# Performance work log

Measured on AMD Instinct MI355X. Metric: run time of the kernel, lower is better.

## Reference

```python
import jax, jax.numpy as jnp
import numpy as np

B, N, D, H, CD = 1, 512, 256, 8, 3
HD = D // H
HID = int(D * 4.0 * (2.0 / 3.0))  # 682, SwiGLU hidden


def _ln(x, w, b, eps=1e-5):
    mu = jnp.mean(x, axis=-1, keepdims=True)
    var = jnp.var(x, axis=-1, keepdims=True)
    return (x - mu) / jnp.sqrt(var + eps) * w + b


def setup_inputs() -> dict:
    key = jax.random.key(0)
    ks = jax.random.split(key, 24)
    g = lambda i, shape, fan: jax.random.normal(ks[i], shape, jnp.float32) * (1.0 / np.sqrt(fan))
    return {
        "x": jax.random.normal(ks[0], (B, N, D), jnp.float32),
        "coords": jax.random.normal(ks[1], (B, N, CD), jnp.float32),
        "ln1_w": jnp.ones((D,), jnp.float32), "ln1_b": jnp.zeros((D,), jnp.float32),
        "ln2_w": jnp.ones((D,), jnp.float32), "ln2_b": jnp.zeros((D,), jnp.float32),
        "qkv_w": g(2, (3 * D, D), D), "qkv_b": jnp.zeros((3 * D,), jnp.float32),
        "rb1_w": g(3, (D, CD), CD), "rb1_b": jnp.zeros((D,), jnp.float32),
        "rb2_w": g(4, (H, D), D), "rb2_b": jnp.zeros((H,), jnp.float32),
        "rv1_w": g(5, (D, CD), CD), "rv1_b": jnp.zeros((D,), jnp.float32),
        "rv2_w": g(6, (D, D), D), "rv2_b": jnp.zeros((D,), jnp.float32),
        "ffn_w1": g(7, (HID, D), D), "ffn_b1": jnp.zeros((HID,), jnp.float32),
        "ffn_w2": g(8, (HID, D), D), "ffn_b2": jnp.zeros((HID,), jnp.float32),
        "ffn_w3": g(9, (D, HID), HID), "ffn_b3": jnp.zeros((D,), jnp.float32),
    }


def _forward(x, coords, ln1_w, ln1_b, ln2_w, ln2_b, qkv_w, qkv_b,
             rb1_w, rb1_b, rb2_w, rb2_b, rv1_w, rv1_b, rv2_w, rv2_b,
             ffn_w1, ffn_b1, ffn_w2, ffn_b2, ffn_w3, ffn_b3):
    silu = jax.nn.silu
    xn = _ln(x, ln1_w, ln1_b)
    qkv = xn @ qkv_w.T + qkv_b                       # [B,N,3D]
    q, k, v = jnp.split(qkv, 3, axis=-1)
    tohead = lambda t: t.reshape(B, N, H, HD).transpose(0, 2, 1, 3)  # [B,H,N,hd]
    qh, kh, vh = tohead(q), tohead(k), tohead(v)

    rel = coords[:, :, None, :] - coords[:, None, :, :]              # [B,N,N,3]
    rel_bias = silu(rel @ rb1_w.T + rb1_b) @ rb2_w.T + rb2_b         # [B,N,N,H]
    rel_bias = rel_bias.transpose(0, 3, 1, 2)                        # [B,H,N,N]
    rel_value = silu(rel @ rv1_w.T + rv1_b) @ rv2_w.T + rv2_b        # [B,N,N,D]
    rel_value = rel_value.reshape(B, N, N, H, HD).transpose(0, 3, 1, 2, 4)  # [B,H,N,N,hd]

    scores = jnp.einsum('bhid,bhjd->bhij', qh, kh) / np.sqrt(float(HD))
    weights = jax.nn.softmax(scores + rel_bias, axis=-1)             # [B,H,N,N]
    context = jnp.einsum('bhij,bhjd->bhid', weights, vh) \
            + jnp.einsum('bhij,bhijd->bhid', weights, rel_value)
    attn_out = context.transpose(0, 2, 1, 3).reshape(B, N, D)

    x = x + attn_out
    xn2 = _ln(x, ln2_w, ln2_b)
    ffn = (silu(xn2 @ ffn_w1.T + ffn_b1) * (xn2 @ ffn_w2.T + ffn_b2)) @ ffn_w3.T + ffn_b3
    return x + ffn


def reference(x, coords, ln1_w, ln1_b, ln2_w, ln2_b, qkv_w, qkv_b,
              rb1_w, rb1_b, rb2_w, rb2_b, rv1_w, rv1_b, rv2_w, rv2_b,
              ffn_w1, ffn_b1, ffn_w2, ffn_b2, ffn_w3, ffn_b3):
    return _forward(x, coords, ln1_w, ln1_b, ln2_w, ln2_b, qkv_w, qkv_b,
                    rb1_w, rb1_b, rb2_w, rb2_b, rv1_w, rv1_b, rv2_w, rv2_b,
                    ffn_w1, ffn_b1, ffn_w2, ffn_b2, ffn_w3, ffn_b3)
```

## Files before the change

kernel.cpp:

```cpp
#include <hip/hip_runtime.h>


#define NN 512
#define DD 256
#define HH 8
#define HIDN 682
#define QKSCALE 0.17677669529663687f

#define OFF_XN     0
#define OFF_X2     0
#define OFF_Q      131072
#define OFF_W3P    131072
#define OFF_VPF    262144
#define OFF_RV2T   393216
#define OFF_RB2F   458752
#define OFF_KF     460800
#define OFF_PBF    526336
#define OFF_H1     526336
#define OFF_PVF    788480
#define OFF_QKVP   1050624
#define OFF_XN2    1050624
#define OFF_W12P   1247232

typedef float  f32x4  __attribute__((ext_vector_type(4)));
typedef short  bf16x8 __attribute__((ext_vector_type(8)));
typedef unsigned int u32;
typedef unsigned short ushortt;

static __device__ __forceinline__ float wredSum(float v){
#pragma unroll
  for (int o = 1; o < 64; o <<= 1) v += __shfl_xor(v, o, 64);
  return v;
}
static __device__ __forceinline__ float wredMax(float v){
#pragma unroll
  for (int o = 1; o < 64; o <<= 1) v = fmaxf(v, __shfl_xor(v, o, 64));
  return v;
}
static __device__ __forceinline__ float fsilu(float x){
  return x * __builtin_amdgcn_rcpf(1.0f + __expf(-x));
}
static __device__ __forceinline__ u32 cvtpk(float lo, float hi){
  u32 d; asm("v_cvt_pk_bf16_f32 %0, %1, %2" : "=v"(d) : "v"(lo), "v"(hi));
  return d;
}
static __device__ __forceinline__ float us2f(ushortt u){
  union{u32 u; float f;} c; c.u = ((u32)u) << 16; return c.f;
}
static __device__ __forceinline__ bf16x8 mkfrag(u32 a, u32 b, u32 c, u32 d){
  union{u32 u[4]; bf16x8 s;} f; f.u[0]=a; f.u[1]=b; f.u[2]=c; f.u[3]=d; return f.s;
}
static __device__ __forceinline__ float dot4(float4 a, float4 b){
  return a.x*b.x + a.y*b.y + a.z*b.z + a.w*b.w;
}

__global__ __launch_bounds__(256) void k1_prep(
    const float* __restrict__ x, const float* __restrict__ coords,
    const float* __restrict__ ln1_w, const float* __restrict__ ln1_b,
    const float* __restrict__ rb1_w, const float* __restrict__ rv1_w,
    const float* __restrict__ rv2_w, const float* __restrict__ rb2_w,
    const float* __restrict__ qkv_w, const float* __restrict__ w1,
    const float* __restrict__ w2, float* __restrict__ ws)
{
  __shared__ float r4[4];
  const int b = blockIdx.x, t = threadIdx.x;
  if (b < 512) {
    const int lane = t & 63, wid = t >> 6;
    const float v = x[b*DD + t];
    float s = wredSum(v);
    if (lane == 0) r4[wid] = s;
    __syncthreads();
    const float mu = (r4[0]+r4[1]+r4[2]+r4[3]) * (1.0f/DD);
    const float d = v - mu;
    float s2 = wredSum(d*d);
    __syncthreads();
    if (lane == 0) r4[wid] = s2;
    __syncthreads();
    const float var = (r4[0]+r4[1]+r4[2]+r4[3]) * (1.0f/DD);
    ws[OFF_XN + b*DD + t] = d*rsqrtf(var + 1e-5f)*ln1_w[t] + ln1_b[t];
  } else if (b < 768) {
    const int e = b - 512;
    ws[OFF_RV2T + e*DD + t] = rv2_w[t*DD + e];
  } else if (b == 768) {
    u32* RBF = (u32*)(ws + OFF_RB2F);
    const int l = t & 63, lm = l & 15, lg = (l >> 4) & 3, kq = t >> 6;
#pragma unroll
    for (int g = 0; g < 2; ++g) {
      const int ks = g*4 + kq;
      u32 dw[4];
#pragma unroll
      for (int dd = 0; dd < 4; ++dd) {
        const int e0 = ks*32 + lg*8 + 2*dd;
        const float f0 = (lm < HH) ? rb2_w[lm*DD + e0]     : 0.f;
        const float f1 = (lm < HH) ? rb2_w[lm*DD + e0 + 1] : 0.f;
        dw[dd] = cvtpk(f0, f1);
      }
      uint4 q4; q4.x = dw[0]; q4.y = dw[1]; q4.z = dw[2]; q4.w = dw[3];
      *(uint4*)(RBF + (ks*64 + l)*4) = q4;
    }
  } else if (b < 833) {
    float4* dst = (float4*)(ws + OFF_PBF);
#pragma unroll
    for (int k = 0; k < 4; ++k) {
      const int L4 = (b - 769)*1024 + k*256 + t;
      const int lm = L4 & 15, q = (L4>>4)&3, lg = (L4>>6)&3, ks = (L4>>8)&7, jt = L4>>11;
      const int j = jt*16 + lm, e0 = ks*32 + lg*8 + q*2;
      const float c0 = coords[j*3], c1 = coords[j*3+1], c2 = coords[j*3+2];
      const float p0 = c0*rb1_w[e0*3]   + c1*rb1_w[e0*3+1] + c2*rb1_w[e0*3+2];
      const float p1 = c0*rb1_w[e0*3+3] + c1*rb1_w[e0*3+4] + c2*rb1_w[e0*3+5];
      dst[L4] = make_float4(p0, __expf(p0), p1, __expf(p1));
    }
  } else if (b < 897) {
    float4* dst = (float4*)(ws + OFF_PVF);
#pragma unroll
    for (int k = 0; k < 4; ++k) {
      const int L4 = (b - 833)*1024 + k*256 + t;
      const int lm = L4 & 15, q = (L4>>4)&3, lg = (L4>>6)&3, ks = (L4>>8)&15, et = L4>>12;
      const int e = et*16 + lm, j0 = ks*32 + lg*8 + q*2;
      const float w0 = rv1_w[e*3], w1_ = rv1_w[e*3+1], w2_ = rv1_w[e*3+2];
      const float p0 = coords[j0*3]*w0 + coords[j0*3+1]*w1_ + coords[j0*3+2]*w2_;
      const float p1 = coords[j0*3+3]*w0 + coords[j0*3+4]*w1_ + coords[j0*3+5]*w2_;
      dst[L4] = make_float4(p0, __expf(p0), p1, __expf(p1));
    }
  } else if (b < 945) {
    float4* dst = (float4*)(ws + OFF_QKVP);
#pragma unroll
    for (int k = 0; k < 4; ++k) {
      const int L4 = (b - 897)*1024 + k*256 + t;
      const int O = L4 % 768, k4 = L4 / 768;
      dst[L4] = *(const float4*)(qkv_w + O*DD + k4*4);
    }
  } else {
    float4* dst = (float4*)(ws + OFF_W12P);
    for (int L4 = (b - 945)*256 + t; L4 < 87296; L4 += 88*256) {
      const int pr = L4 & 1, rest = L4 >> 1;
      const int O = rest % 682, k4 = rest / 682;
      dst[L4] = *(const float4*)((pr ? w2 : w1) + O*DD + k4*4);
    }
  }
}

__global__ __launch_bounds__(256) void k2_qkv(
    float* __restrict__ ws, const float* __restrict__ qkv_b)
{
  const int i0 = blockIdx.x*2, rep = blockIdx.y, t = threadIdx.x;
  const int O = rep*DD + t;
  const float4* xn4 = (const float4*)(ws + OFF_XN);
  const float4* wp4 = (const float4*)(ws + OFF_QKVP);
  float a0 = qkv_b[O], a1 = a0;
  for (int k4 = 0; k4 < 64; ++k4) {
    const float4 w = wp4[k4*768 + O];
    const float4 x0 = xn4[i0*64 + k4];
    const float4 x1 = xn4[i0*64 + 64 + k4];
    a0 += dot4(x0, w);
    a1 += dot4(x1, w);
  }
  if (rep == 0) {
    ws[OFF_Q + i0*DD + t] = a0;
    ws[OFF_Q + (i0+1)*DD + t] = a1;
  } else if (rep == 1) {
    u32* KF = (u32*)(ws + OFF_KF);
    const int c = t;
    const float p0 = __shfl_xor(a0, 1);
    const float p1 = __shfl_xor(a1, 1);
    if ((c & 1) == 0) {
      const int hq = c >> 5, lgk = (c >> 3) & 3, dw = (c & 7) >> 1;
      const int jt0_ = i0 >> 4, lm0 = i0 & 15;
      KF[(((jt0_*8 + hq)*4 + lgk)*16 + lm0)*4 + dw] = cvtpk(a0, p0);
      const int j1 = i0 + 1, jt1_ = j1 >> 4, lm1 = j1 & 15;
      KF[(((jt1_*8 + hq)*4 + lgk)*16 + lm1)*4 + dw] = cvtpk(a1, p1);
    }
  } else {
    ws[OFF_VPF + i0*DD + t] = a0;
    ws[OFF_VPF + (i0+1)*DD + t] = a1;
  }
}

__global__ __launch_bounds__(512, 4) void k3_attn(
    const float* __restrict__ x, const float* __restrict__ coords,
    const float* __restrict__ rb1_w, const float* __restrict__ rb1_b,
    const float* __restrict__ rv1_w, const float* __restrict__ rv1_b,
    const float* __restrict__ rv2_b, const float* __restrict__ ln2_w,
    const float* __restrict__ ln2_b, float* __restrict__ ws)
{
  __shared__ __align__(16) float aI[DD], eIl[DD], pvIl[DD], evIl[DD], qI[DD];
  __shared__ __align__(16) float uni[4352];
  __shared__ __align__(16) float GhL[HH*258];
  __shared__ __align__(16) float c1h[2*DD];
  __shared__ float red[8];
  float* swl = uni;
  ushortt* wtl = (ushortt*)uni;

  const int i = blockIdx.x, t = threadIdx.x;
  const int lane = t & 63, wid = t >> 6, lm = lane & 15, lg = lane >> 4;
  const float* qbuf = ws + OFF_Q;
  const float4* PBF4 = (const float4*)(ws + OFF_PBF);
  const float4* PVF4 = (const float4*)(ws + OFF_PVF);
  const uint4*  KF4  = (const uint4*)(ws + OFF_KF);
  const u32*    RBF  = (const u32*)(ws + OFF_RB2F);
  const float*  rv2t = ws + OFF_RV2T;
  const float*  vpf  = ws + OFF_VPF;

  if (t < DD) {
    const float c0 = coords[i*3], c1 = coords[i*3+1], c2 = coords[i*3+2];
    const float a  = c0*rb1_w[t*3] + c1*rb1_w[t*3+1] + c2*rb1_w[t*3+2] + rb1_b[t];
    aI[t] = a;  eIl[t] = __expf(-a);
    const float pv = c0*rv1_w[t*3] + c1*rv1_w[t*3+1] + c2*rv1_w[t*3+2] + rv1_b[t];
    pvIl[t] = pv; evIl[t] = __expf(-pv);
    qI[t] = qbuf[i*DD + t];
  }
  __syncthreads();

  {
    f32x4 z4 = {0.f,0.f,0.f,0.f};
    f32x4 acc[4] = {z4,z4,z4,z4};
    const int jt0 = wid*4;
    for (int ks = 0; ks < 8; ++ks) {
      const uint4 bd = *(const uint4*)(RBF + (ks*64 + lane)*4);
      const bf16x8 bfr = mkfrag(bd.x, bd.y, bd.z, bd.w);
      const float4 aA0 = *(const float4*)&aI[ks*32 + lg*8];
      const float4 aA1 = *(const float4*)&aI[ks*32 + lg*8 + 4];
      const float4 eA0 = *(const float4*)&eIl[ks*32 + lg*8];
      const float4 eA1 = *(const float4*)&eIl[ks*32 + lg*8 + 4];
#pragma unroll
      for (int jt = 0; jt < 4; ++jt) {
        const float4* src = PBF4 + ((jt0+jt)*32 + ks*4 + lg)*64 + lm;
        const float4 g0 = src[0], g1 = src[16], g2 = src[32], g3 = src[48];
        const float s0 = (aA0.x-g0.x)*__builtin_amdgcn_rcpf(fmaf(eA0.x,g0.y,1.f));
        const float s1 = (aA0.y-g0.z)*__builtin_amdgcn_rcpf(fmaf(eA0.y,g0.w,1.f));
        const float s2 = (aA0.z-g1.x)*__builtin_amdgcn_rcpf(fmaf(eA0.z,g1.y,1.f));
        const float s3 = (aA0.w-g1.z)*__builtin_amdgcn_rcpf(fmaf(eA0.w,g1.w,1.f));
        const float s4 = (aA1.x-g2.x)*__builtin_amdgcn_rcpf(fmaf(eA1.x,g2.y,1.f));
        const float s5 = (aA1.y-g2.z)*__builtin_amdgcn_rcpf(fmaf(eA1.y,g2.w,1.f));
        const float s6 = (aA1.z-g3.x)*__builtin_amdgcn_rcpf(fmaf(eA1.z,g3.y,1.f));
        const float s7 = (aA1.w-g3.z)*__builtin_amdgcn_rcpf(fmaf(eA1.w,g3.w,1.f));
        const bf16x8 afr = mkfrag(cvtpk(s0,s1), cvtpk(s2,s3), cvtpk(s4,s5), cvtpk(s6,s7));
        acc[jt] = __builtin_amdgcn_mfma_f32_16x16x32_bf16(afr, bfr, acc[jt], 0, 0, 0);
      }
    }
#pragma unroll
    for (int hq = 0; hq < 8; ++hq) {
      const float4 q0 = *(const float4*)&qI[hq*32 + lg*8];
      const float4 q1 = *(const float4*)&qI[hq*32 + lg*8 + 4];
      const float m = (lm == hq) ? QKSCALE : 0.f;
      const bf16x8 bfr = mkfrag(cvtpk(q0.x*m, q0.y*m), cvtpk(q0.z*m, q0.w*m),
                                cvtpk(q1.x*m, q1.y*m), cvtpk(q1.z*m, q1.w*m));
#pragma unroll
      for (int jt = 0; jt < 4; ++jt) {
        const uint4 ad = KF4[(((jt0+jt)*8 + hq)*4 + lg)*16 + lm];
        const bf16x8 afr = mkfrag(ad.x, ad.y, ad.z, ad.w);
        acc[jt] = __builtin_amdgcn_mfma_f32_16x16x32_bf16(afr, bfr, acc[jt], 0, 0, 0);
      }
    }
    if (lm < HH) {
#pragma unroll
      for (int jt = 0; jt < 4; ++jt)
#pragma unroll
        for (int g = 0; g < 4; ++g)
          swl[lm*513 + wid*64 + jt*16 + lg*4 + g] = acc[jt][g];
    }
  }
  __syncthreads();

  float sv[8];
  {
    float mm = -3.4e38f;
#pragma unroll
    for (int r = 0; r < 8; ++r) { sv[r] = swl[wid*513 + lane + r*64]; mm = fmaxf(mm, sv[r]); }
    mm = wredMax(mm);
    float sum = 0.f;
#pragma unroll
    for (int r = 0; r < 8; ++r) { sv[r] = __expf(sv[r] - mm); sum += sv[r]; }
    sum = wredSum(sum);
    const float rz = __builtin_amdgcn_rcpf(sum);
#pragma unroll
    for (int r = 0; r < 8; ++r) sv[r] *= rz;
  }
  __syncthreads();
#pragma unroll
  for (int r = 0; r < 8; ++r)
    wtl[(lane + r*64)*17 + wid] = (ushortt)(cvtpk(sv[r], 0.f) & 0xFFFFu);
  __syncthreads();

  {
    f32x4 z4 = {0.f,0.f,0.f,0.f};
    f32x4 accB0 = z4, accB1 = z4;
    const int et0 = wid*2;
    const int eR0 = et0*16 + lm, eR1 = eR0 + 16;
    const float aV0 = pvIl[eR0], eV0 = evIl[eR0];
    const float aV1 = pvIl[eR1], eV1 = evIl[eR1];
    for (int ks = 0; ks < 16; ++ks) {
      ushortt wv[8];
#pragma unroll
      for (int r = 0; r < 8; ++r) wv[r] = wtl[(ks*32 + lg*8 + r)*17 + lm];
      const bf16x8 wfr = mkfrag((u32)wv[0] | ((u32)wv[1] << 16),
                                (u32)wv[2] | ((u32)wv[3] << 16),
                                (u32)wv[4] | ((u32)wv[5] << 16),
                                (u32)wv[6] | ((u32)wv[7] << 16));
      {
        const float4* src = PVF4 + ((et0*16 + ks)*4 + lg)*64 + lm;
        const float4 g0 = src[0], g1 = src[16], g2 = src[32], g3 = src[48];
        const float s0 = (aV0-g0.x)*__builtin_amdgcn_rcpf(fmaf(eV0,g0.y,1.f));
        const float s1 = (aV0-g0.z)*__builtin_amdgcn_rcpf(fmaf(eV0,g0.w,1.f));
        const float s2 = (aV0-g1.x)*__builtin_amdgcn_rcpf(fmaf(eV0,g1.y,1.f));
        const float s3 = (aV0-g1.z)*__builtin_amdgcn_rcpf(fmaf(eV0,g1.w,1.f));
        const float s4 = (aV0-g2.x)*__builtin_amdgcn_rcpf(fmaf(eV0,g2.y,1.f));
        const float s5 = (aV0-g2.z)*__builtin_amdgcn_rcpf(fmaf(eV0,g2.w,1.f));
        const float s6 = (aV0-g3.x)*__builtin_amdgcn_rcpf(fmaf(eV0,g3.y,1.f));
        const float s7 = (aV0-g3.z)*__builtin_amdgcn_rcpf(fmaf(eV0,g3.w,1.f));
        const bf16x8 afr = mkfrag(cvtpk(s0,s1), cvtpk(s2,s3), cvtpk(s4,s5), cvtpk(s6,s7));
        accB0 = __builtin_amdgcn_mfma_f32_16x16x32_bf16(afr, wfr, accB0, 0, 0, 0);
      }
      {
        const float4* src = PVF4 + (((et0+1)*16 + ks)*4 + lg)*64 + lm;
        const float4 g0 = src[0], g1 = src[16], g2 = src[32], g3 = src[48];
        const float s0 = (aV1-g0.x)*__builtin_amdgcn_rcpf(fmaf(eV1,g0.y,1.f));
        const float s1 = (aV1-g0.z)*__builtin_amdgcn_rcpf(fmaf(eV1,g0.w,1.f));
        const float s2 = (aV1-g1.x)*__builtin_amdgcn_rcpf(fmaf(eV1,g1.y,1.f));
        const float s3 = (aV1-g1.z)*__builtin_amdgcn_rcpf(fmaf(eV1,g1.w,1.f));
        const float s4 = (aV1-g2.x)*__builtin_amdgcn_rcpf(fmaf(eV1,g2.y,1.f));
        const float s5 = (aV1-g2.z)*__builtin_amdgcn_rcpf(fmaf(eV1,g2.w,1.f));
        const float s6 = (aV1-g3.x)*__builtin_amdgcn_rcpf(fmaf(eV1,g3.y,1.f));
        const float s7 = (aV1-g3.z)*__builtin_amdgcn_rcpf(fmaf(eV1,g3.w,1.f));
        const bf16x8 afr = mkfrag(cvtpk(s0,s1), cvtpk(s2,s3), cvtpk(s4,s5), cvtpk(s6,s7));
        accB1 = __builtin_amdgcn_mfma_f32_16x16x32_bf16(afr, wfr, accB1, 0, 0, 0);
      }
    }
    if (lm < HH) {
#pragma unroll
      for (int g = 0; g < 4; ++g) {
        GhL[lm*258 + et0*16 + lg*4 + g]     = accB0[g];
        GhL[lm*258 + (et0+1)*16 + lg*4 + g] = accB1[g];
      }
    }
  }

  {
    const int c = t & 255, half = t >> 8, h = c >> 5;
    float a0 = 0.f;
    for (int j = half*256; j < half*256 + 256; ++j)
      a0 += us2f(wtl[j*17 + h]) * vpf[j*DD + c];
    c1h[half*DD + c] = a0;
  }
  __syncthreads();

  float x2v = 0.f;
  if (t < DD) {
    const int c = t, h = c >> 5;
    float a0 = 0.f;
    for (int e = 0; e < DD; ++e) a0 += GhL[h*258 + e] * rv2t[e*DD + c];
    x2v = x[i*DD + c] + c1h[c] + c1h[DD + c] + a0 + rv2_b[c];
  }
  float s = wredSum(x2v);
  if (lane == 0) red[wid] = s;
  __syncthreads();
  const float mu = (red[0]+red[1]+red[2]+red[3]) * (1.0f/DD);
  const float dv = (t < DD) ? (x2v - mu) : 0.f;
  float s2 = wredSum(dv*dv);
  __syncthreads();
  if (lane == 0) red[wid] = s2;
  __syncthreads();
  const float var = (red[0]+red[1]+red[2]+red[3]) * (1.0f/DD);
  const float rstd = rsqrtf(var + 1e-5f);
  if (t < DD) {
    ws[OFF_X2  + i*DD + t] = x2v;
    ws[OFF_XN2 + i*DD + t] = (x2v - mu)*rstd*ln2_w[t] + ln2_b[t];
  }
}

__global__ __launch_bounds__(256) void k4_ffn1(
    float* __restrict__ ws, const float* __restrict__ b1,
    const float* __restrict__ b2, const float* __restrict__ w3)
{
  const int rep = blockIdx.y, t = threadIdx.x;
  if (rep == 3) {
    float2* dst = (float2*)(ws + OFF_W3P);
    for (int L2 = blockIdx.x*256 + t; L2 < 87296; L2 += 256*256) {
      const int c = L2 & 255, k2i = L2 >> 8;
      dst[L2] = *(const float2*)(w3 + c*HIDN + 2*k2i);
    }
    return;
  }
  const int i0 = blockIdx.x*2;
  const int O = rep*DD + t;
  if (O >= HIDN) return;
  const float4* xn4 = (const float4*)(ws + OFF_XN2);
  const float4* wp4 = (const float4*)(ws + OFF_W12P);
  float a10 = b1[O], a11 = a10;
  float a20 = b2[O], a21 = a20;
  for (int k4 = 0; k4 < 64; ++k4) {
    const float4 u = wp4[(k4*HIDN + O)*2];
    const float4 v = wp4[(k4*HIDN + O)*2 + 1];
    const float4 x0 = xn4[i0*64 + k4];
    const float4 x1 = xn4[i0*64 + 64 + k4];
    a10 += dot4(x0, u); a20 += dot4(x0, v);
    a11 += dot4(x1, u); a21 += dot4(x1, v);
  }
  ws[OFF_H1 + i0*HIDN + O]     = fsilu(a10)*a20;
  ws[OFF_H1 + (i0+1)*HIDN + O] = fsilu(a11)*a21;
}

__global__ __launch_bounds__(256) void k5_ffn2(
    const float* __restrict__ ws, const float* __restrict__ b3, float* __restrict__ out)
{
  const int i = blockIdx.x, c = threadIdx.x;
  const float2* wp2 = (const float2*)(ws + OFF_W3P);
  const float2* h2  = (const float2*)(ws + OFF_H1 + i*HIDN);
  float acc = b3[c] + ws[OFF_X2 + i*DD + c];
  for (int k = 0; k < 341; ++k) {
    const float2 w = wp2[k*DD + c];
    const float2 h = h2[k];
    acc += h.x*w.x + h.y*w.y;
  }
  out[i*DD + c] = acc;
}

extern "C" void kernel_launch(void* const* d_in, const int* in_sizes, int n_in,
                              void* d_out, int out_size, void* d_ws, size_t ws_size,
                              hipStream_t stream) {
  (void)in_sizes; (void)n_in; (void)out_size; (void)ws_size;
  const float* x      = (const float*)d_in[0];
  const float* coords = (const float*)d_in[1];
  const float* ln1_w  = (const float*)d_in[2];
  const float* ln1_b  = (const float*)d_in[3];
  const float* ln2_w  = (const float*)d_in[4];
  const float* ln2_b  = (const float*)d_in[5];
  const float* qkv_w  = (const float*)d_in[6];
  const float* qkv_b  = (const float*)d_in[7];
  const float* rb1_w  = (const float*)d_in[8];
  const float* rb1_b  = (const float*)d_in[9];
  const float* rb2_w  = (const float*)d_in[10];
  const float* rv1_w  = (const float*)d_in[12];
  const float* rv1_b  = (const float*)d_in[13];
  const float* rv2_w  = (const float*)d_in[14];
  const float* rv2_b  = (const float*)d_in[15];
  const float* ffn_w1 = (const float*)d_in[16];
  const float* ffn_b1 = (const float*)d_in[17];
  const float* ffn_w2 = (const float*)d_in[18];
  const float* ffn_b2 = (const float*)d_in[19];
  const float* ffn_w3 = (const float*)d_in[20];
  const float* ffn_b3 = (const float*)d_in[21];
  float* ws  = (float*)d_ws;
  float* out = (float*)d_out;

  k1_prep<<<1033, 256, 0, stream>>>(x, coords, ln1_w, ln1_b, rb1_w, rv1_w,
                                    rv2_w, rb2_w, qkv_w, ffn_w1, ffn_w2, ws);
  k2_qkv<<<dim3(256, 3), 256, 0, stream>>>(ws, qkv_b);
  k3_attn<<<NN, 512, 0, stream>>>(x, coords, rb1_w, rb1_b, rv1_w, rv1_b, rv2_b,
                                  ln2_w, ln2_b, ws);
  k4_ffn1<<<dim3(256, 4), 256, 0, stream>>>(ws, ffn_b1, ffn_b2, ffn_w3);
  k5_ffn2<<<NN, 256, 0, stream>>>(ws, ffn_b3, out);
}
```

Before: 259.6 us.

## Split attention into scores, softmax, context kernels with fp16 packing and row blocking

The monolithic per-row attention kernel becomes three kernels. The first computes bias and QK scores for four query rows per block, sharing fragment loads across rows. The second applies softmax over packed fp16 weights, and the third computes the value and rel-value context for two rows per block, doing the rv2 projection with MFMA instead of a scalar loop. Precomputed coordinate projections are stored as fp16 without the exp half, Q is pre-scaled into bf16, V is stored transposed in bf16, and the FFN weight packing moves to its own kernel. The FFN kernels now process 16 rows per block so each weight load is reused across rows. This adds launches and lowers intermediate precision, which risks larger numerical error.

After: 336.8 us. 1.3x slower.

```diff
diff --git a/kernel.cpp b/kernel.cpp
--- a/kernel.cpp
+++ b/kernel.cpp
@@ -7,25 +7,26 @@
 #define HIDN 682
 #define QKSCALE 0.17677669529663687f
 
-#define OFF_XN     0
-#define OFF_X2     0
-#define OFF_Q      131072
-#define OFF_W3P    131072
-#define OFF_VPF    262144
-#define OFF_RV2T   393216
-#define OFF_RB2F   458752
-#define OFF_KF     460800
-#define OFF_PBF    526336
-#define OFF_H1     526336
-#define OFF_PVF    788480
-#define OFF_QKVP   1050624
-#define OFF_XN2    1050624
-#define OFF_W12P   1247232
+#define OFF_QB    0
+#define OFF_PB    65536
+#define OFF_X2    0
+#define OFF_KF    131072
+#define OFF_RB2F  196608
+#define OFF_XN2   131072
+#define OFF_RV2F  262144
+#define OFF_VT    294912
+#define OFF_PV    360448
+#define OFF_WB    425984
+#define OFF_XN    425984
+#define OFF_QKVP  557056
+#define OFF_W12P  425984
+#define OFF_W3P   775168
+#define OFF_H1    949760
 
 typedef float  f32x4  __attribute__((ext_vector_type(4)));
 typedef short  bf16x8 __attribute__((ext_vector_type(8)));
+typedef __fp16 fp16x2 __attribute__((ext_vector_type(2)));
 typedef unsigned int u32;
-typedef unsigned short ushortt;
 
 static __device__ __forceinline__ float wredSum(float v){
 #pragma unroll
@@ -44,8 +45,15 @@
   u32 d; asm("v_cvt_pk_bf16_f32 %0, %1, %2" : "=v"(d) : "v"(lo), "v"(hi));
   return d;
 }
-static __device__ __forceinline__ float us2f(ushortt u){
-  union{u32 u; float f;} c; c.u = ((u32)u) << 16; return c.f;
+static __device__ __forceinline__ u32 pkf16(float lo, float hi){
+  fp16x2 r = __builtin_amdgcn_cvt_pkrtz(lo, hi);
+  union{fp16x2 h; u32 u;} c; c.h = r; return c.u;
+}
+static __device__ __forceinline__ float f16lo(u32 d){
+  union{unsigned short s; __fp16 h;} c; c.s = (unsigned short)(d & 0xffffu); return (float)c.h;
+}
+static __device__ __forceinline__ float f16hi(u32 d){
+  union{unsigned short s; __fp16 h;} c; c.s = (unsigned short)(d >> 16); return (float)c.h;
 }
 static __device__ __forceinline__ bf16x8 mkfrag(u32 a, u32 b, u32 c, u32 d){
   union{u32 u[4]; bf16x8 s;} f; f.u[0]=a; f.u[1]=b; f.u[2]=c; f.u[3]=d; return f.s;
@@ -59,8 +67,7 @@
     const float* __restrict__ ln1_w, const float* __restrict__ ln1_b,
     const float* __restrict__ rb1_w, const float* __restrict__ rv1_w,
     const float* __restrict__ rv2_w, const float* __restrict__ rb2_w,
-    const float* __restrict__ qkv_w, const float* __restrict__ w1,
-    const float* __restrict__ w2, float* __restrict__ ws)
+    const float* __restrict__ qkv_w, float* __restrict__ ws)
 {
   __shared__ float r4[4];
   const int b = blockIdx.x, t = threadIdx.x;
@@ -78,64 +85,78 @@
     __syncthreads();
     const float var = (r4[0]+r4[1]+r4[2]+r4[3]) * (1.0f/DD);
     ws[OFF_XN + b*DD + t] = d*rsqrtf(var + 1e-5f)*ln1_w[t] + ln1_b[t];
-  } else if (b < 768) {
-    const int e = b - 512;
-    ws[OFF_RV2T + e*DD + t] = rv2_w[t*DD + e];
-  } else if (b == 768) {
+  } else if (b < 528) {
+    u32* PB32 = (u32*)(ws + OFF_PB);
+#pragma unroll
+    for (int k = 0; k < 4; ++k) {
+      const int L = (b-512)*1024 + k*256 + t;
+      const int jt = L >> 9, ks = (L >> 6) & 7, ln = L & 63;
+      const int lmm = ln & 15, lgg = ln >> 4;
+      const int j = jt*16 + lmm, e0 = ks*32 + lgg*8;
+      const float c0 = coords[j*3], c1 = coords[j*3+1], c2 = coords[j*3+2];
+      float p[8];
+#pragma unroll
+      for (int r = 0; r < 8; ++r)
+        p[r] = c0*rb1_w[(e0+r)*3] + c1*rb1_w[(e0+r)*3+1] + c2*rb1_w[(e0+r)*3+2];
+      uint4 q; q.x = pkf16(p[0],p[1]); q.y = pkf16(p[2],p[3]);
+      q.z = pkf16(p[4],p[5]); q.w = pkf16(p[6],p[7]);
+      *(uint4*)(PB32 + (size_t)L*4) = q;
+    }
+  } else if (b < 544) {
+    u32* PV32 = (u32*)(ws + OFF_PV);
+#pragma unroll
+    for (int k = 0; k < 4; ++k) {
+      const int L = (b-528)*1024 + k*256 + t;
+      const int et = L >> 10, ks = (L >> 6) & 15, ln = L & 63;
+      const int lmm = ln & 15, lgg = ln >> 4;
+      const int e = et*16 + lmm, j0 = ks*32 + lgg*8;
+      const float w0 = rv1_w[e*3], w1 = rv1_w[e*3+1], w2 = rv1_w[e*3+2];
+      float p[8];
+#pragma unroll
+      for (int r = 0; r < 8; ++r)
+        p[r] = coords[(j0+r)*3]*w0 + coords[(j0+r)*3+1]*w1 + coords[(j0+r)*3+2]*w2;
+      uint4 q; q.x = pkf16(p[0],p[1]); q.y = pkf16(p[2],p[3]);
+      q.z = pkf16(p[4],p[5]); q.w = pkf16(p[6],p[7]);
+      *(uint4*)(PV32 + (size_t)L*4) = q;
+    }
+  } else if (b < 552) {
+    u32* RV32 = (u32*)(ws + OFF_RV2F);
+#pragma unroll
+    for (int k = 0; k < 4; ++k) {
+      const int L = (b-544)*1024 + k*256 + t;
+      const int mt = L >> 9, ks2 = (L >> 6) & 7, ln = L & 63;
+      const int lmm = ln & 15, lgg = ln >> 4;
+      const int c = mt*16 + lmm, e0 = ks2*32 + lgg*8;
+      const float4 f0 = *(const float4*)(rv2_w + c*DD + e0);
+      const float4 f1 = *(const float4*)(rv2_w + c*DD + e0 + 4);
+      uint4 q; q.x = cvtpk(f0.x,f0.y); q.y = cvtpk(f0.z,f0.w);
+      q.z = cvtpk(f1.x,f1.y); q.w = cvtpk(f1.z,f1.w);
+      *(uint4*)(RV32 + (size_t)L*4) = q;
+    }
+  } else if (b == 552) {
     u32* RBF = (u32*)(ws + OFF_RB2F);
-    const int l = t & 63, lm = l & 15, lg = (l >> 4) & 3, kq = t >> 6;
+    const int l = t & 63, lmm = l & 15, lgg = (l >> 4) & 3, kq = t >> 6;
 #pragma unroll
     for (int g = 0; g < 2; ++g) {
       const int ks = g*4 + kq;
       u32 dw[4];
 #pragma unroll
       for (int dd = 0; dd < 4; ++dd) {
-        const int e0 = ks*32 + lg*8 + 2*dd;
-        const float f0 = (lm < HH) ? rb2_w[lm*DD + e0]     : 0.f;
-        const float f1 = (lm < HH) ? rb2_w[lm*DD + e0 + 1] : 0.f;
+        const int e0 = ks*32 + lgg*8 + 2*dd;
+        const float f0 = (lmm < HH) ? rb2_w[lmm*DD + e0]     : 0.f;
+        const float f1 = (lmm < HH) ? rb2_w[lmm*DD + e0 + 1] : 0.f;
         dw[dd] = cvtpk(f0, f1);
       }
       uint4 q4; q4.x = dw[0]; q4.y = dw[1]; q4.z = dw[2]; q4.w = dw[3];
       *(uint4*)(RBF + (ks*64 + l)*4) = q4;
     }
-  } else if (b < 833) {
-    float4* dst = (float4*)(ws + OFF_PBF);
+  } else {
+    float4* dst = (float4*)(ws + OFF_QKVP);
 #pragma unroll
     for (int k = 0; k < 4; ++k) {
-      const int L4 = (b - 769)*1024 + k*256 + t;
-      const int lm = L4 & 15, q = (L4>>4)&3, lg = (L4>>6)&3, ks = (L4>>8)&7, jt = L4>>11;
-      const int j = jt*16 + lm, e0 = ks*32 + lg*8 + q*2;
-      const float c0 = coords[j*3], c1 = coords[j*3+1], c2 = coords[j*3+2];
-      const float p0 = c0*rb1_w[e0*3]   + c1*rb1_w[e0*3+1] + c2*rb1_w[e0*3+2];
-      const float p1 = c0*rb1_w[e0*3+3] + c1*rb1_w[e0*3+4] + c2*rb1_w[e0*3+5];
-      dst[L4] = make_float4(p0, __expf(p0), p1, __expf(p1));
-    }
-  } else if (b < 897) {
-    float4* dst = (float4*)(ws + OFF_PVF);
-#pragma unroll
-    for (int k = 0; k < 4; ++k) {
-      const int L4 = (b - 833)*1024 + k*256 + t;
-      const int lm = L4 & 15, q = (L4>>4)&3, lg = (L4>>6)&3, ks = (L4>>8)&15, et = L4>>12;
-      const int e = et*16 + lm, j0 = ks*32 + lg*8 + q*2;
-      const float w0 = rv1_w[e*3], w1_ = rv1_w[e*3+1], w2_ = rv1_w[e*3+2];
-      const float p0 = coords[j0*3]*w0 + coords[j0*3+1]*w1_ + coords[j0*3+2]*w2_;
-      const float p1 = coords[j0*3+3]*w0 + coords[j0*3+4]*w1_ + coords[j0*3+5]*w2_;
-      dst[L4] = make_float4(p0, __expf(p0), p1, __expf(p1));
-    }
-  } else if (b < 945) {
-    float4* dst = (float4*)(ws + OFF_QKVP);
-#pragma unroll
-    for (int k = 0; k < 4; ++k) {
-      const int L4 = (b - 897)*1024 + k*256 + t;
+      const int L4 = (b - 553)*1024 + k*256 + t;
       const int O = L4 % 768, k4 = L4 / 768;
       dst[L4] = *(const float4*)(qkv_w + O*DD + k4*4);
-    }
-  } else {
-    float4* dst = (float4*)(ws + OFF_W12P);
-    for (int L4 = (b - 945)*256 + t; L4 < 87296; L4 += 88*256) {
-      const int pr = L4 & 1, rest = L4 >> 1;
-      const int O = rest % 682, k4 = rest / 682;
-      dst[L4] = *(const float4*)((pr ? w2 : w1) + O*DD + k4*4);
     }
   }
 }
@@ -156,263 +177,349 @@
     a1 += dot4(x1, w);
   }
   if (rep == 0) {
-    ws[OFF_Q + i0*DD + t] = a0;
-    ws[OFF_Q + (i0+1)*DD + t] = a1;
+    u32* QB = (u32*)(ws + OFF_QB);
+    const float s0 = a0*QKSCALE, s1 = a1*QKSCALE;
+    const float p0 = __shfl_xor(s0, 1);
+    const float p1 = __shfl_xor(s1, 1);
+    if ((t & 1) == 0) {
+      QB[i0*128 + (t >> 1)]     = cvtpk(s0, p0);
+      QB[(i0+1)*128 + (t >> 1)] = cvtpk(s1, p1);
+    }
   } else if (rep == 1) {
     u32* KF = (u32*)(ws + OFF_KF);
-    const int c = t;
     const float p0 = __shfl_xor(a0, 1);
     const float p1 = __shfl_xor(a1, 1);
-    if ((c & 1) == 0) {
-      const int hq = c >> 5, lgk = (c >> 3) & 3, dw = (c & 7) >> 1;
+    if ((t & 1) == 0) {
+      const int hq = t >> 5, lgk = (t >> 3) & 3, dw = (t & 7) >> 1;
       const int jt0_ = i0 >> 4, lm0 = i0 & 15;
       KF[(((jt0_*8 + hq)*4 + lgk)*16 + lm0)*4 + dw] = cvtpk(a0, p0);
       const int j1 = i0 + 1, jt1_ = j1 >> 4, lm1 = j1 & 15;
       KF[(((jt1_*8 + hq)*4 + lgk)*16 + lm1)*4 + dw] = cvtpk(a1, p1);
     }
   } else {
-    ws[OFF_VPF + i0*DD + t] = a0;
-    ws[OFF_VPF + (i0+1)*DD + t] = a1;
-  }
-}
-
-__global__ __launch_bounds__(512, 4) void k3_attn(
+    u32* VT = (u32*)(ws + OFF_VT);
+    VT[t*256 + (i0 >> 1)] = cvtpk(a0, a1);
+  }
+}
+
+__global__ __launch_bounds__(256, 2) void k3a_scores(
+    const float* __restrict__ coords, const float* __restrict__ rb1_w,
+    const float* __restrict__ rb1_b, float* __restrict__ ws)
+{
+  __shared__ __align__(16) float aI4[4][DD];
+  __shared__ __align__(16) float eI4[4][DD];
+  const int bx = blockIdx.x, t = threadIdx.x;
+  const int it = bx >> 2, jq = bx & 3, i0 = it*4;
+  const int lane = t & 63, w = t >> 6, lm = lane & 15, lg = lane >> 4;
+  {
+    const float w0 = rb1_w[t*3], w1 = rb1_w[t*3+1], w2 = rb1_w[t*3+2], bb = rb1_b[t];
+#pragma unroll
+    for (int i = 0; i < 4; ++i) {
+      const float a = coords[(i0+i)*3]*w0 + coords[(i0+i)*3+1]*w1
+                    + coords[(i0+i)*3+2]*w2 + bb;
+      aI4[i][t] = a; eI4[i][t] = __expf(-a);
+    }
+  }
+  __syncthreads();
+  const uint4* PBu = (const uint4*)(ws + OFF_PB);
+  const uint4* KFu = (const uint4*)(ws + OFF_KF);
+  const uint4* QBu = (const uint4*)(ws + OFF_QB);
+  const u32*   RBF = (const u32*)(ws + OFF_RB2F);
+  const int jtA = jq*8 + w*2;
+  f32x4 z = {0,0,0,0};
+  f32x4 acc[2][4] = {{z,z,z,z},{z,z,z,z}};
+  for (int ks = 0; ks < 8; ++ks) {
+    const uint4 bd = *(const uint4*)(RBF + (ks*64 + lane)*4);
+    const bf16x8 bfr = mkfrag(bd.x,bd.y,bd.z,bd.w);
+    float4 aA[4][2], eA[4][2];
+#pragma unroll
+    for (int i = 0; i < 4; ++i) {
+      aA[i][0] = *(const float4*)&aI4[i][ks*32 + lg*8];
+      aA[i][1] = *(const float4*)&aI4[i][ks*32 + lg*8 + 4];
+      eA[i][0] = *(const float4*)&eI4[i][ks*32 + lg*8];
+      eA[i][1] = *(const float4*)&eI4[i][ks*32 + lg*8 + 4];
+    }
+#pragma unroll
+    for (int j2 = 0; j2 < 2; ++j2) {
+      const uint4 pd = PBu[((jtA+j2)*8 + ks)*64 + lane];
+      float p[8], ep[8];
+      p[0]=f16lo(pd.x); p[1]=f16hi(pd.x); p[2]=f16lo(pd.y); p[3]=f16hi(pd.y);
+      p[4]=f16lo(pd.z); p[5]=f16hi(pd.z); p[6]=f16lo(pd.w); p[7]=f16hi(pd.w);
+#pragma unroll
+      for (int r = 0; r < 8; ++r) ep[r] = __expf(p[r]);
+#pragma unroll
+      for (int i = 0; i < 4; ++i) {
+        const float* aa = (const float*)&aA[i][0];
+        const float* ee = (const float*)&eA[i][0];
+        float s[8];
+#pragma unroll
+        for (int r = 0; r < 8; ++r)
+          s[r] = (aa[r] - p[r]) * __builtin_amdgcn_rcpf(fmaf(ee[r], ep[r], 1.f));
+        const bf16x8 afr = mkfrag(cvtpk(s[0],s[1]), cvtpk(s[2],s[3]),
+                                  cvtpk(s[4],s[5]), cvtpk(s[6],s[7]));
+        acc[j2][i] = __builtin_amdgcn_mfma_f32_16x16x32_bf16(afr, bfr, acc[j2][i], 0,0,0);
+      }
+    }
+  }
+#pragma unroll
+  for (int hq = 0; hq < 8; ++hq) {
+    uint4 qd[4];
+#pragma unroll
+    for (int i = 0; i < 4; ++i) qd[i] = QBu[(i0+i)*32 + hq*4 + lg];
+    const bool sel = (lm == hq);
+#pragma unroll
+    for (int j2 = 0; j2 < 2; ++j2) {
+      const uint4 kd = KFu[((jtA+j2)*8 + hq)*64 + lane];
+      const bf16x8 kfr = mkfrag(kd.x,kd.y,kd.z,kd.w);
+#pragma unroll
+      for (int i = 0; i < 4; ++i) {
+        const bf16x8 qfr = mkfrag(sel?qd[i].x:0u, sel?qd[i].y:0u,
+                                  sel?qd[i].z:0u, sel?qd[i].w:0u);
+        acc[j2][i] = __builtin_amdgcn_mfma_f32_16x16x32_bf16(kfr, qfr, acc[j2][i], 0,0,0);
+      }
+    }
+  }
+  u32* WB = (u32*)(ws + OFF_WB);
+  if (lm < HH) {
+#pragma unroll
+    for (int j2 = 0; j2 < 2; ++j2) {
+      const int jt = jtA + j2, j0 = jt*16 + lg*4;
+      const int ksw = j0 >> 5, rr = j0 & 31, lgw = rr >> 3, d0 = (rr & 7) >> 1;
+#pragma unroll
+      for (int i = 0; i < 4; ++i) {
+        const int idx = (((i0+i)*16 + ksw)*32 + lgw*8 + lm)*4 + d0;
+        uint2 st; st.x = pkf16(acc[j2][i][0], acc[j2][i][1]);
+        st.y = pkf16(acc[j2][i][2], acc[j2][i][3]);
+        *(uint2*)(WB + idx) = st;
+      }
+    }
+  }
+}
+
+__global__ __launch_bounds__(256) void k3b_softmax(float* __restrict__ ws)
+{
+  const int i = blockIdx.x, t = threadIdx.x;
+  const int lane = t & 63, w4 = t >> 6;
+  u32* WB = (u32*)(ws + OFF_WB);
+  const int ks = lane >> 2, d = lane & 3;
+#pragma unroll
+  for (int hh = 0; hh < 2; ++hh) {
+    const int h = w4 + hh*4;
+    u32 dv[4]; float v[8];
+#pragma unroll
+    for (int lg = 0; lg < 4; ++lg) {
+      dv[lg] = WB[(i*16 + ks)*128 + (lg*8 + h)*4 + d];
+      v[lg*2]   = f16lo(dv[lg]);
+      v[lg*2+1] = f16hi(dv[lg]);
+    }
+    float m = v[0];
+#pragma unroll
+    for (int r = 1; r < 8; ++r) m = fmaxf(m, v[r]);
+    m = wredMax(m);
+    float s = 0.f;
+#pragma unroll
+    for (int r = 0; r < 8; ++r) { v[r] = __expf(v[r] - m); s += v[r]; }
+    s = wredSum(s);
+    const float rz = __builtin_amdgcn_rcpf(s);
+#pragma unroll
+    for (int lg = 0; lg < 4; ++lg)
+      WB[(i*16 + ks)*128 + (lg*8 + h)*4 + d] = cvtpk(v[lg*2]*rz, v[lg*2+1]*rz);
+  }
+}
+
+__global__ __launch_bounds__(512, 2) void k3c_ctx(
     const float* __restrict__ x, const float* __restrict__ coords,
-    const float* __restrict__ rb1_w, const float* __restrict__ rb1_b,
     const float* __restrict__ rv1_w, const float* __restrict__ rv1_b,
     const float* __restrict__ rv2_b, const float* __restrict__ ln2_w,
     const float* __restrict__ ln2_b, float* __restrict__ ws)
 {
-  __shared__ __align__(16) float aI[DD], eIl[DD], pvIl[DD], evIl[DD], qI[DD];
-  __shared__ __align__(16) float uni[4352];
-  __shared__ __align__(16) float GhL[HH*258];
-  __shared__ __align__(16) float c1h[2*DD];
-  __shared__ float red[8];
-  float* swl = uni;
-  ushortt* wtl = (ushortt*)uni;
-
-  const int i = blockIdx.x, t = threadIdx.x;
-  const int lane = t & 63, wid = t >> 6, lm = lane & 15, lg = lane >> 4;
-  const float* qbuf = ws + OFF_Q;
-  const float4* PBF4 = (const float4*)(ws + OFF_PBF);
-  const float4* PVF4 = (const float4*)(ws + OFF_PVF);
-  const uint4*  KF4  = (const uint4*)(ws + OFF_KF);
-  const u32*    RBF  = (const u32*)(ws + OFF_RB2F);
-  const float*  rv2t = ws + OFF_RV2T;
-  const float*  vpf  = ws + OFF_VPF;
-
-  if (t < DD) {
-    const float c0 = coords[i*3], c1 = coords[i*3+1], c2 = coords[i*3+2];
-    const float a  = c0*rb1_w[t*3] + c1*rb1_w[t*3+1] + c2*rb1_w[t*3+2] + rb1_b[t];
-    aI[t] = a;  eIl[t] = __expf(-a);
-    const float pv = c0*rv1_w[t*3] + c1*rv1_w[t*3+1] + c2*rv1_w[t*3+2] + rv1_b[t];
-    pvIl[t] = pv; evIl[t] = __expf(-pv);
-    qI[t] = qbuf[i*DD + t];
-  }
-  __syncthreads();
-
+  __shared__ __align__(16) float aV2[2][DD];
+  __shared__ __align__(16) float eV2[2][DD];
+  __shared__ __align__(16) float Gs[2][HH][260];
+  __shared__ __align__(16) float x2t[2][257];
+  __shared__ float red[2][4];
+  const int bx = blockIdx.x, t = threadIdx.x, i0 = bx*2;
+  const int lane = t & 63, w = t >> 6, lm = lane & 15, lg = lane >> 4;
   {
-    f32x4 z4 = {0.f,0.f,0.f,0.f};
-    f32x4 acc[4] = {z4,z4,z4,z4};
-    const int jt0 = wid*4;
-    for (int ks = 0; ks < 8; ++ks) {
-      const uint4 bd = *(const uint4*)(RBF + (ks*64 + lane)*4);
-      const bf16x8 bfr = mkfrag(bd.x, bd.y, bd.z, bd.w);
-      const float4 aA0 = *(const float4*)&aI[ks*32 + lg*8];
-      const float4 aA1 = *(const float4*)&aI[ks*32 + lg*8 + 4];
-      const float4 eA0 = *(const float4*)&eIl[ks*32 + lg*8];
-      const float4 eA1 = *(const float4*)&eIl[ks*32 + lg*8 + 4];
-#pragma unroll
-      for (int jt = 0; jt < 4; ++jt) {
-        const float4* src = PBF4 + ((jt0+jt)*32 + ks*4 + lg)*64 + lm;
-        const float4 g0 = src[0], g1 = src[16], g2 = src[32], g3 = src[48];
-        const float s0 = (aA0.x-g0.x)*__builtin_amdgcn_rcpf(fmaf(eA0.x,g0.y,1.f));
-        const float s1 = (aA0.y-g0.z)*__builtin_amdgcn_rcpf(fmaf(eA0.y,g0.w,1.f));
-        const float s2 = (aA0.z-g1.x)*__builtin_amdgcn_rcpf(fmaf(eA0.z,g1.y,1.f));
-        const float s3 = (aA0.w-g1.z)*__builtin_amdgcn_rcpf(fmaf(eA0.w,g1.w,1.f));
-        const float s4 = (aA1.x-g2.x)*__builtin_amdgcn_rcpf(fmaf(eA1.x,g2.y,1.f));
-        const float s5 = (aA1.y-g2.z)*__builtin_amdgcn_rcpf(fmaf(eA1.y,g2.w,1.f));
-        const float s6 = (aA1.z-g3.x)*__builtin_amdgcn_rcpf(fmaf(eA1.z,g3.y,1.f));
-        const float s7 = (aA1.w-g3.z)*__builtin_amdgcn_rcpf(fmaf(eA1.w,g3.w,1.f));
-        const bf16x8 afr = mkfrag(cvtpk(s0,s1), cvtpk(s2,s3), cvtpk(s4,s5), cvtpk(s6,s7));
-        acc[jt] = __builtin_amdgcn_mfma_f32_16x16x32_bf16(afr, bfr, acc[jt], 0, 0, 0);
+    const int ii = t >> 8, e = t & 255;
+    const float pv = coords[(i0+ii)*3]*rv1_w[e*3] + coords[(i0+ii)*3+1]*rv1_w[e*3+1]
+                   + coords[(i0+ii)*3+2]*rv1_w[e*3+2] + rv1_b[e];
+    aV2[ii][e] = pv; eV2[ii][e] = __expf(-pv);
+  }
+  __syncthreads();
+  const uint4* WBu = (const uint4*)(ws + OFF_WB);
+  const uint4* PVu = (const uint4*)(ws + OFF_PV);
+  const uint4* VTu = (const uint4*)(ws + OFF_VT);
+  const uint4* RVu = (const uint4*)(ws + OFF_RV2F);
+  f32x4 z = {0,0,0,0};
+  f32x4 accg[2][2] = {{z,z},{z,z}};
+  f32x4 ac1[2] = {z,z};
+  float aV[2][2], eV[2][2];
+#pragma unroll
+  for (int e2 = 0; e2 < 2; ++e2)
+#pragma unroll
+    for (int ig = 0; ig < 2; ++ig) {
+      aV[e2][ig] = aV2[ig][(w*2+e2)*16 + lm];
+      eV[e2][ig] = eV2[ig][(w*2+e2)*16 + lm];
+    }
+  for (int ks = 0; ks < 16; ++ks) {
+    bf16x8 wfr[2];
+#pragma unroll
+    for (int ig = 0; ig < 2; ++ig) {
+      const uint4 wd = WBu[((i0+ig)*16 + ks)*32 + lg*8 + lm];
+      wfr[ig] = mkfrag(wd.x,wd.y,wd.z,wd.w);
+    }
+    const uint4 cd = WBu[((i0+lm)*16 + ks)*32 + lg*8 + w];
+    const bf16x8 c1b = mkfrag(cd.x,cd.y,cd.z,cd.w);
+#pragma unroll
+    for (int e2 = 0; e2 < 2; ++e2) {
+      const int et = w*2 + e2;
+      const uint4 pd = PVu[(et*16 + ks)*64 + lane];
+      float p[8], ep[8];
+      p[0]=f16lo(pd.x); p[1]=f16hi(pd.x); p[2]=f16lo(pd.y); p[3]=f16hi(pd.y);
+      p[4]=f16lo(pd.z); p[5]=f16hi(pd.z); p[6]=f16lo(pd.w); p[7]=f16hi(pd.w);
+#pragma unroll
+      for (int r = 0; r < 8; ++r) ep[r] = __expf(p[r]);
+#pragma unroll
+      for (int ig = 0; ig < 2; ++ig) {
+        float s[8];
+#pragma unroll
+        for (int r = 0; r < 8; ++r)
+          s[r] = (aV[e2][ig] - p[r]) * __builtin_amdgcn_rcpf(fmaf(eV[e2][ig], ep[r], 1.f));
+        const bf16x8 afr = mkfrag(cvtpk(s[0],s[1]), cvtpk(s[2],s[3]),
+                                  cvtpk(s[4],s[5]), cvtpk(s[6],s[7]));
+        accg[e2][ig] = __builtin_amdgcn_mfma_f32_16x16x32_bf16(afr, wfr[ig], accg[e2][ig], 0,0,0);
       }
     }
 #pragma unroll
-    for (int hq = 0; hq < 8; ++hq) {
-      const float4 q0 = *(const float4*)&qI[hq*32 + lg*8];
-      const float4 q1 = *(const float4*)&qI[hq*32 + lg*8 + 4];
-      const float m = (lm == hq) ? QKSCALE : 0.f;
-      const bf16x8 bfr = mkfrag(cvtpk(q0.x*m, q0.y*m), cvtpk(q0.z*m, q0.w*m),
-                                cvtpk(q1.x*m, q1.y*m), cvtpk(q1.z*m, q1.w*m));
-#pragma unroll
-      for (int jt = 0; jt < 4; ++jt) {
-        const uint4 ad = KF4[(((jt0+jt)*8 + hq)*4 + lg)*16 + lm];
-        const bf16x8 afr = mkfrag(ad.x, ad.y, ad.z, ad.w);
-        acc[jt] = __builtin_amdgcn_mfma_f32_16x16x32_bf16(afr, bfr, acc[jt], 0, 0, 0);
-      }
-    }
-    if (lm < HH) {
-#pragma unroll
-      for (int jt = 0; jt < 4; ++jt)
+    for (int m2 = 0; m2 < 2; ++m2) {
+      const int c = (w*2 + m2)*16 + lm;
+      const uint4 vd = VTu[c*64 + ks*4 + lg];
+      const bf16x8 vfr = mkfrag(vd.x,vd.y,vd.z,vd.w);
+      ac1[m2] = __builtin_amdgcn_mfma_f32_16x16x32_bf16(vfr, c1b, ac1[m2], 0,0,0);
+    }
+  }
+  if (lm < HH) {
+#pragma unroll
+    for (int e2 = 0; e2 < 2; ++e2)
+#pragma unroll
+      for (int ig = 0; ig < 2; ++ig)
 #pragma unroll
         for (int g = 0; g < 4; ++g)
-          swl[lm*513 + wid*64 + jt*16 + lg*4 + g] = acc[jt][g];
-    }
-  }
-  __syncthreads();
-
-  float sv[8];
-  {
-    float mm = -3.4e38f;
-#pragma unroll
-    for (int r = 0; r < 8; ++r) { sv[r] = swl[wid*513 + lane + r*64]; mm = fmaxf(mm, sv[r]); }
-    mm = wredMax(mm);
-    float sum = 0.f;
-#pragma unroll
-    for (int r = 0; r < 8; ++r) { sv[r] = __expf(sv[r] - mm); sum += sv[r]; }
-    sum = wredSum(sum);
-    const float rz = __builtin_amdgcn_rcpf(sum);
-#pragma unroll
-    for (int r = 0; r < 8; ++r) sv[r] *= rz;
-  }
-  __syncthreads();
-#pragma unroll
-  for (int r = 0; r < 8; ++r)
-    wtl[(lane + r*64)*17 + wid] = (ushortt)(cvtpk(sv[r], 0.f) & 0xFFFFu);
-  __syncthreads();
-
-  {
-    f32x4 z4 = {0.f,0.f,0.f,0.f};
-    f32x4 accB0 = z4, accB1 = z4;
-    const int et0 = wid*2;
-    const int eR0 = et0*16 + lm, eR1 = eR0 + 16;
-    const float aV0 = pvIl[eR0], eV0 = evIl[eR0];
-    const float aV1 = pvIl[eR1], eV1 = evIl[eR1];
-    for (int ks = 0; ks < 16; ++ks) {
-      ushortt wv[8];
-#pragma unroll
-      for (int r = 0; r < 8; ++r) wv[r] = wtl[(ks*32 + lg*8 + r)*17 + lm];
-      const bf16x8 wfr = mkfrag((u32)wv[0] | ((u32)wv[1] << 16),
-                                (u32)wv[2] | ((u32)wv[3] << 16),
-                                (u32)wv[4] | ((u32)wv[5] << 16),
-                                (u32)wv[6] | ((u32)wv[7] << 16));
-      {
-        const float4* src = PVF4 + ((et0*16 + ks)*4 + lg)*64 + lm;
-        const float4 g0 = src[0], g1 = src[16], g2 = src[32], g3 = src[48];
-        const float s0 = (aV0-g0.x)*__builtin_amdgcn_rcpf(fmaf(eV0,g0.y,1.f));
-        const float s1 = (aV0-g0.z)*__builtin_amdgcn_rcpf(fmaf(eV0,g0.w,1.f));
-        const float s2 = (aV0-g1.x)*__builtin_amdgcn_rcpf(fmaf(eV0,g1.y,1.f));
-        const float s3 = (aV0-g1.z)*__builtin_amdgcn_rcpf(fmaf(eV0,g1.w,1.f));
-        const float s4 = (aV0-g2.x)*__builtin_amdgcn_rcpf(fmaf(eV0,g2.y,1.f));
-        const float s5 = (aV0-g2.z)*__builtin_amdgcn_rcpf(fmaf(eV0,g2.w,1.f));
-        const float s6 = (aV0-g3.x)*__builtin_amdgcn_rcpf(fmaf(eV0,g3.y,1.f));
-        const float s7 = (aV0-g3.z)*__builtin_amdgcn_rcpf(fmaf(eV0,g3.w,1.f));
-        const bf16x8 afr = mkfrag(cvtpk(s0,s1), cvtpk(s2,s3), cvtpk(s4,s5), cvtpk(s6,s7));
-        accB0 = __builtin_amdgcn_mfma_f32_16x16x32_bf16(afr, wfr, accB0, 0, 0, 0);
-      }
-      {
-        const float4* src = PVF4 + (((et0+1)*16 + ks)*4 + lg)*64 + lm;
-        const float4 g0 = src[0], g1 = src[16], g2 = src[32], g3 = src[48];
-        const float s0 = (aV1-g0.x)*__builtin_amdgcn_rcpf(fmaf(eV1,g0.y,1.f));
-        const float s1 = (aV1-g0.z)*__builtin_amdgcn_rcpf(fmaf(eV1,g0.w,1.f));
-        const float s2 = (aV1-g1.x)*__builtin_amdgcn_rcpf(fmaf(eV1,g1.y,1.f));
-        const float s3 = (aV1-g1.z)*__builtin_amdgcn_rcpf(fmaf(eV1,g1.w,1.f));
-        const float s4 = (aV1-g2.x)*__builtin_amdgcn_rcpf(fmaf(eV1,g2.y,1.f));
-        const float s5 = (aV1-g2.z)*__builtin_amdgcn_rcpf(fmaf(eV1,g2.w,1.f));
-        const float s6 = (aV1-g3.x)*__builtin_amdgcn_rcpf(fmaf(eV1,g3.y,1.f));
-        const float s7 = (aV1-g3.z)*__builtin_amdgcn_rcpf(fmaf(eV1,g3.w,1.f));
-        const bf16x8 afr = mkfrag(cvtpk(s0,s1), cvtpk(s2,s3), cvtpk(s4,s5), cvtpk(s6,s7));
-        accB1 = __builtin_amdgcn_mfma_f32_16x16x32_bf16(afr, wfr, accB1, 0, 0, 0);
-      }
-    }
-    if (lm < HH) {
-#pragma unroll
-      for (int g = 0; g < 4; ++g) {
-        GhL[lm*258 + et0*16 + lg*4 + g]     = accB0[g];
-        GhL[lm*258 + (et0+1)*16 + lg*4 + g] = accB1[g];
-      }
-    }
-  }
-
-  {
-    const int c = t & 255, half = t >> 8, h = c >> 5;
-    float a0 = 0.f;
-    for (int j = half*256; j < half*256 + 256; ++j)
-      a0 += us2f(wtl[j*17 + h]) * vpf[j*DD + c];
-    c1h[half*DD + c] = a0;
-  }
-  __syncthreads();
-
-  float x2v = 0.f;
-  if (t < DD) {
-    const int c = t, h = c >> 5;
-    float a0 = 0.f;
-    for (int e = 0; e < DD; ++e) a0 += GhL[h*258 + e] * rv2t[e*DD + c];
-    x2v = x[i*DD + c] + c1h[c] + c1h[DD + c] + a0 + rv2_b[c];
-  }
-  float s = wredSum(x2v);
-  if (lane == 0) red[wid] = s;
-  __syncthreads();
-  const float mu = (red[0]+red[1]+red[2]+red[3]) * (1.0f/DD);
-  const float dv = (t < DD) ? (x2v - mu) : 0.f;
+          Gs[ig][lm][(w*2+e2)*16 + lg*4 + g] = accg[e2][ig][g];
+  }
+  __syncthreads();
+  f32x4 ac2[2] = {z,z};
+  const int il = lm & 1;
+  for (int k2 = 0; k2 < 8; ++k2) {
+    const float4 g0 = *(const float4*)&Gs[il][w][k2*32 + lg*8];
+    const float4 g1 = *(const float4*)&Gs[il][w][k2*32 + lg*8 + 4];
+    const bf16x8 gfr = mkfrag(cvtpk(g0.x,g0.y), cvtpk(g0.z,g0.w),
+                              cvtpk(g1.x,g1.y), cvtpk(g1.z,g1.w));
+#pragma unroll
+    for (int m2 = 0; m2 < 2; ++m2) {
+      const uint4 ad = RVu[((w*2+m2)*8 + k2)*64 + lane];
+      const bf16x8 afr = mkfrag(ad.x,ad.y,ad.z,ad.w);
+      ac2[m2] = __builtin_amdgcn_mfma_f32_16x16x32_bf16(afr, gfr, ac2[m2], 0,0,0);
+    }
+  }
+#pragma unroll
+  for (int m2 = 0; m2 < 2; ++m2) {
+    const int c0 = (w*2 + m2)*16 + lg*4;
+    const float4 rb = *(const float4*)(rv2_b + c0);
+    if (lm < 2) {
+      const float4 xv = *(const float4*)(x + (i0+lm)*DD + c0);
+      x2t[lm][c0+0] = ac1[m2][0] + ac2[m2][0] + rb.x + xv.x;
+      x2t[lm][c0+1] = ac1[m2][1] + ac2[m2][1] + rb.y + xv.y;
+      x2t[lm][c0+2] = ac1[m2][2] + ac2[m2][2] + rb.z + xv.z;
+      x2t[lm][c0+3] = ac1[m2][3] + ac2[m2][3] + rb.w + xv.w;
+    }
+  }
+  __syncthreads();
+  const int ii = t >> 8, c = t & 255;
+  const float v = x2t[ii][c];
+  float s1 = wredSum(v);
+  if (lane == 0) red[ii][w & 3] = s1;
+  __syncthreads();
+  const float mu = (red[ii][0]+red[ii][1]+red[ii][2]+red[ii][3]) * (1.0f/DD);
+  const float dv = v - mu;
   float s2 = wredSum(dv*dv);
   __syncthreads();
-  if (lane == 0) red[wid] = s2;
-  __syncthreads();
-  const float var = (red[0]+red[1]+red[2]+red[3]) * (1.0f/DD);
+  if (lane == 0) red[ii][w & 3] = s2;
+  __syncthreads();
+  const float var = (red[ii][0]+red[ii][1]+red[ii][2]+red[ii][3]) * (1.0f/DD);
   const float rstd = rsqrtf(var + 1e-5f);
-  if (t < DD) {
-    ws[OFF_X2  + i*DD + t] = x2v;
-    ws[OFF_XN2 + i*DD + t] = (x2v - mu)*rstd*ln2_w[t] + ln2_b[t];
-  }
-}
-
-__global__ __launch_bounds__(256) void k4_ffn1(
-    float* __restrict__ ws, const float* __restrict__ b1,
-    const float* __restrict__ b2, const float* __restrict__ w3)
-{
-  const int rep = blockIdx.y, t = threadIdx.x;
-  if (rep == 3) {
+  ws[OFF_X2  + (i0+ii)*DD + c] = v;
+  ws[OFF_XN2 + (i0+ii)*DD + c] = dv*rstd*ln2_w[c] + ln2_b[c];
+}
+
+__global__ __launch_bounds__(256) void k3p_pack(
+    const float* __restrict__ w1, const float* __restrict__ w2,
+    const float* __restrict__ w3, float* __restrict__ ws)
+{
+  const int b = blockIdx.x, t = threadIdx.x;
+  if (b < 88) {
+    float4* dst = (float4*)(ws + OFF_W12P);
+    for (int L4 = b*256 + t; L4 < 87296; L4 += 88*256) {
+      const int pr = L4 & 1, rest = L4 >> 1;
+      const int O = rest % 682, k4 = rest / 682;
+      dst[L4] = *(const float4*)((pr ? w2 : w1) + O*DD + k4*4);
+    }
+  } else {
     float2* dst = (float2*)(ws + OFF_W3P);
-    for (int L2 = blockIdx.x*256 + t; L2 < 87296; L2 += 256*256) {
+    for (int L2 = (b-88)*256 + t; L2 < 87296; L2 += 44*256) {
       const int c = L2 & 255, k2i = L2 >> 8;
       dst[L2] = *(const float2*)(w3 + c*HIDN + 2*k2i);
     }
-    return;
-  }
-  const int i0 = blockIdx.x*2;
+  }
+}
+
+__global__ __launch_bounds__(256) void k4_ffn1(
+    float* __restrict__ ws, const float* __restrict__ b1, const float* __restrict__ b2)
+{
+  const int i0 = blockIdx.x*16, rep = blockIdx.y, t = threadIdx.x;
   const int O = rep*DD + t;
   if (O >= HIDN) return;
   const float4* xn4 = (const float4*)(ws + OFF_XN2);
   const float4* wp4 = (const float4*)(ws + OFF_W12P);
-  float a10 = b1[O], a11 = a10;
-  float a20 = b2[O], a21 = a20;
+  float a1[16], a2[16];
+  const float bb1 = b1[O], bb2 = b2[O];
+#pragma unroll
+  for (int r = 0; r < 16; ++r) { a1[r] = bb1; a2[r] = bb2; }
   for (int k4 = 0; k4 < 64; ++k4) {
     const float4 u = wp4[(k4*HIDN + O)*2];
     const float4 v = wp4[(k4*HIDN + O)*2 + 1];
-    const float4 x0 = xn4[i0*64 + k4];
-    const float4 x1 = xn4[i0*64 + 64 + k4];
-    a10 += dot4(x0, u); a20 += dot4(x0, v);
-    a11 += dot4(x1, u); a21 += dot4(x1, v);
-  }
-  ws[OFF_H1 + i0*HIDN + O]     = fsilu(a10)*a20;
-  ws[OFF_H1 + (i0+1)*HIDN + O] = fsilu(a11)*a21;
-}
-
-__global__ __launch_bounds__(256) void k5_ffn2(
+#pragma unroll
+    for (int r = 0; r < 16; ++r) {
+      const float4 xv = xn4[(i0+r)*64 + k4];
+      a1[r] += dot4(xv, u); a2[r] += dot4(xv, v);
+    }
+  }
+#pragma unroll
+  for (int r = 0; r < 16; ++r)
+    ws[OFF_H1 + (size_t)(i0+r)*HIDN + O] = fsilu(a1[r]) * a2[r];
+}
+
+__global__ __launch_bounds__(128) void k5_ffn2(
     const float* __restrict__ ws, const float* __restrict__ b3, float* __restrict__ out)
 {
-  const int i = blockIdx.x, c = threadIdx.x;
+  const int i0 = blockIdx.x*16, ch = blockIdx.y, t = threadIdx.x;
+  const int c = ch*128 + t;
   const float2* wp2 = (const float2*)(ws + OFF_W3P);
-  const float2* h2  = (const float2*)(ws + OFF_H1 + i*HIDN);
-  float acc = b3[c] + ws[OFF_X2 + i*DD + c];
+  float acc[16];
+  const float bb = b3[c];
+#pragma unroll
+  for (int r = 0; r < 16; ++r) acc[r] = bb + ws[OFF_X2 + (i0+r)*DD + c];
   for (int k = 0; k < 341; ++k) {
-    const float2 w = wp2[k*DD + c];
-    const float2 h = h2[k];
-    acc += h.x*w.x + h.y*w.y;
-  }
-  out[i*DD + c] = acc;
+    const float2 wv = wp2[k*DD + c];
+#pragma unroll
+    for (int r = 0; r < 16; ++r) {
+      const float2 hv = *(const float2*)(ws + OFF_H1 + (size_t)(i0+r)*HIDN + 2*k);
+      acc[r] += hv.x*wv.x + hv.y*wv.y;
+    }
+  }
+#pragma unroll
+  for (int r = 0; r < 16; ++r) out[(i0+r)*DD + c] = acc[r];
 }
 
 extern "C" void kernel_launch(void* const* d_in, const int* in_sizes, int n_in,
@@ -443,11 +550,13 @@
   float* ws  = (float*)d_ws;
   float* out = (float*)d_out;
 
-  k1_prep<<<1033, 256, 0, stream>>>(x, coords, ln1_w, ln1_b, rb1_w, rv1_w,
-                                    rv2_w, rb2_w, qkv_w, ffn_w1, ffn_w2, ws);
+  k1_prep<<<601, 256, 0, stream>>>(x, coords, ln1_w, ln1_b, rb1_w, rv1_w,
+                                   rv2_w, rb2_w, qkv_w, ws);
   k2_qkv<<<dim3(256, 3), 256, 0, stream>>>(ws, qkv_b);
-  k3_attn<<<NN, 512, 0, stream>>>(x, coords, rb1_w, rb1_b, rv1_w, rv1_b, rv2_b,
-                                  ln2_w, ln2_b, ws);
-  k4_ffn1<<<dim3(256, 4), 256, 0, stream>>>(ws, ffn_b1, ffn_b2, ffn_w3);
-  k5_ffn2<<<NN, 256, 0, stream>>>(ws, ffn_b3, out);
-}
+  k3a_scores<<<512, 256, 0, stream>>>(coords, rb1_w, rb1_b, ws);
+  k3b_softmax<<<512, 256, 0, stream>>>(ws);
+  k3c_ctx<<<256, 512, 0, stream>>>(x, coords, rv1_w, rv1_b, rv2_b, ln2_w, ln2_b, ws);
+  k3p_pack<<<132, 256, 0, stream>>>(ffn_w1, ffn_w2, ffn_w3, ws);
+  k4_ffn1<<<dim3(32, 3), 256, 0, stream>>>(ws, ffn_b1, ffn_b2);
+  k5_ffn2<<<dim3(32, 2), 128, 0, stream>>>(ws, ffn_b3, out);
+}
```
